# Performance work log

Hardware: AMD Instinct MI355X
Metric: run time of the kernel (lower is better)

Reference implementation:

```python
import jax, jax.numpy as jnp
import numpy as np

TOKENS = 64
IN_F = 8192
OUT_F = 8192
CODESZ = 8
CB_SIZE = 256


def fwht(x):
    """Sylvester fast Walsh-Hadamard transform along last dim. x: (B, n), n power of 2."""
    b, n = x.shape
    h = 1
    while h < n:
        x = x.reshape(b, n // (2 * h), 2, h)
        x = jnp.concatenate([x[:, :, :1] + x[:, :, 1:], x[:, :, :1] - x[:, :, 1:]], axis=2)
        x = x.reshape(b, n)
        h *= 2
    return x


def setup_inputs() -> dict:
    key = jax.random.key(0)
    k0, k1, k2, k3, k4, k5 = jax.random.split(key, 6)
    x = jax.random.normal(k0, (TOKENS, IN_F), jnp.float32)
    # SU/SV are random sign vectors in QuIP
    SU = jnp.sign(jax.random.normal(k1, (IN_F,), jnp.float32))
    SV = jnp.sign(jax.random.normal(k2, (OUT_F,), jnp.float32))
    grid = jax.random.normal(k3, (CB_SIZE, CODESZ), jnp.float32)  # codebook entries
    Wscale = jnp.ones((1,), jnp.float32)
    bias = jax.random.normal(k4, (OUT_F,), jnp.float32) * 0.01
    Qidxs = jax.random.randint(k5, (OUT_F, IN_F // CODESZ), 0, CB_SIZE, jnp.int32)
    return {"x": x, "SU": SU, "SV": SV, "grid": grid, "Wscale": Wscale, "bias": bias, "Qidxs": Qidxs}


def reference(x, SU, SV, grid, Wscale, bias, Qidxs):
    # 1) input sign scale
    xs = x * SU
    # 2) matmul_hadUt with folded wscale: x @ H^T / sqrt(n_in) * wscale (H symmetric Sylvester)
    inv_sqrt_in = 1.0 / jnp.sqrt(jnp.asarray(IN_F, x.dtype))
    xh = fwht(xs) * (inv_sqrt_in * Wscale[0])
    # 3) codebook dequant + matmul: W_hat[o, i] from codebook lookup, out = xh @ W_hat^T
    W_hat = grid[Qidxs].reshape(OUT_F, IN_F)  # (out, in) dequantized weight
    y = xh @ W_hat.T  # (tokens, out)
    # 4) matmul_hadU on the output side, truncate to out_features (no-op here: q_out == out)
    inv_sqrt_out = 1.0 / jnp.sqrt(jnp.asarray(OUT_F, x.dtype))
    yh = fwht(y) * inv_sqrt_out
    yh = yh[..., :OUT_F]
    # 5) output sign scale + bias
    return yh * SV + bias
```

## Files before the change

kernel.cpp:

```cpp
#include <hip/hip_runtime.h>
#include <hip/hip_bf16.h>

#define TOKENS 64
#define IN_F 8192
#define OUT_F 8192
#define CB 256

typedef _Float16 half8 __attribute__((ext_vector_type(8)));
typedef float f32x4 __attribute__((ext_vector_type(4)));

__global__ __launch_bounds__(256) void k_fwht_in(const float* __restrict__ x,
                                                 const float* __restrict__ SU,
                                                 const float* __restrict__ Wscale,
                                                 _Float16* __restrict__ xh_frag)
{
    __shared__ float buf[256 * 33];
    __shared__ _Float16 xrowP[256 * 40];
    const int t    = threadIdx.x;
    const int lane = t & 63;
    const int w    = t >> 6;
    const int row  = blockIdx.x;

    float v[32];
    const float* xr = x + row * IN_F;
#pragma unroll
    for (int r = 0; r < 32; ++r) {
        int e = r * 256 + t;
        v[r] = xr[e] * SU[e];
    }
#pragma unroll
    for (int h = 1; h < 32; h <<= 1) {
#pragma unroll
        for (int r = 0; r < 32; ++r) {
            if ((r & h) == 0) {
                float a = v[r], b = v[r + h];
                v[r] = a + b;
                v[r + h] = a - b;
            }
        }
    }
#pragma unroll
    for (int m = 1; m < 64; m <<= 1) {
        bool upper = (lane & m) != 0;
#pragma unroll
        for (int r = 0; r < 32; ++r) {
            float p = __shfl_xor(v[r], m, 64);
            v[r] = upper ? (p - v[r]) : (v[r] + p);
        }
    }
#pragma unroll
    for (int r = 0; r < 32; ++r) buf[t * 33 + r] = v[r];
    __syncthreads();
    {
        float s1 = (w & 1) ? -1.f : 1.f;
        float s2 = (w & 2) ? -1.f : 1.f;
        float s3 = s1 * s2;
#pragma unroll
        for (int r = 0; r < 32; ++r) {
            float a0 = buf[(0 * 64 + lane) * 33 + r];
            float a1 = buf[(1 * 64 + lane) * 33 + r];
            float a2 = buf[(2 * 64 + lane) * 33 + r];
            float a3 = buf[(3 * 64 + lane) * 33 + r];
            v[r] = a0 + s1 * a1 + s2 * a2 + s3 * a3;
        }
    }
    const float scale = 0.011048543456039806f * Wscale[0];
#pragma unroll
    for (int r = 0; r < 32; ++r) {
        int idx = (t & 31) + (r * 8 + (t >> 5)) * 40;
        xrowP[idx] = (_Float16)(v[r] * scale);
    }
    __syncthreads();
    {
        const int mt  = row >> 4;
        const int l15 = row & 15;
        _Float16* base = xh_frag + ((size_t)(t * 4 + mt) * 64 + l15) * 8;
#pragma unroll
        for (int g = 0; g < 4; ++g) {
            half8 val = *(const half8*)&xrowP[t * 40 + g * 8];
            *(half8*)(base + g * 16 * 8) = val;
        }
    }
}

#define SQ_STRIDE 261
__global__ __launch_bounds__(256, 2) void k_qgemm(const _Float16* __restrict__ xh_frag,
                                                  const int* __restrict__ Qidxs,
                                                  const float* __restrict__ grid,
                                                  float* __restrict__ y_part)
{
    __shared__ __align__(16) _Float16 glds[CB * 8];
    __shared__ __align__(16) char uni[4 * 64 * 68 * 4];
    int*   sq  = (int*)uni;
    float* red = (float*)uni;

    const int tid = threadIdx.x;
    const int g   = blockIdx.x >> 2;
    const int p   = blockIdx.x & 3;
    const int n0  = g * 64;

    {
        const float4* gp = (const float4*)grid + tid * 2;
        float4 g0 = gp[0];
        float4 g1 = gp[1];
        _Float16* gl = &glds[tid * 8];
        gl[0] = (_Float16)g0.x; gl[1] = (_Float16)g0.y;
        gl[2] = (_Float16)g0.z; gl[3] = (_Float16)g0.w;
        gl[4] = (_Float16)g1.x; gl[5] = (_Float16)g1.y;
        gl[6] = (_Float16)g1.z; gl[7] = (_Float16)g1.w;
    }
#pragma unroll
    for (int i = 0; i < 16; ++i) {
        int idx4 = i * 256 + tid;
        int r  = idx4 >> 6;
        int c4 = idx4 & 63;
        int4 vv = *(const int4*)(Qidxs + (size_t)(n0 + r) * 1024 + p * 256 + c4 * 4);
        int* dst = &sq[r * SQ_STRIDE + c4 * 4];
        dst[0] = vv.x; dst[1] = vv.y; dst[2] = vv.z; dst[3] = vv.w;
    }
    __syncthreads();

    const int lane = tid & 63;
    const int w    = tid >> 6;
    const int col  = lane & 15;
    const int quad = lane >> 4;

    const int cbase = w * 64 + quad;
#define QGATHER(dst4, s)                                              \
    {                                                                 \
        int cc = cbase + (s) * 4;                                     \
        dst4.x = sq[(0 * 16 + col) * SQ_STRIDE + cc];                 \
        dst4.y = sq[(1 * 16 + col) * SQ_STRIDE + cc];                 \
        dst4.z = sq[(2 * 16 + col) * SQ_STRIDE + cc];                 \
        dst4.w = sq[(3 * 16 + col) * SQ_STRIDE + cc];                 \
    }

    const _Float16* abase = xh_frag + ((size_t)(p * 64 + w * 16) * 4 * 64 + lane) * 8;

    f32x4 acc[4][4] = {};

    int4 qv1, qv2;
    half8 b_c[4];
    {
        int4 qv0;
        QGATHER(qv0, 0);
        QGATHER(qv1, 1);
        QGATHER(qv2, 2);
        b_c[0] = *(const half8*)&glds[qv0.x * 8];
        b_c[1] = *(const half8*)&glds[qv0.y * 8];
        b_c[2] = *(const half8*)&glds[qv0.z * 8];
        b_c[3] = *(const half8*)&glds[qv0.w * 8];
    }
    half8 a_c[4], a_n[4];
#pragma unroll
    for (int mt = 0; mt < 4; ++mt) {
        a_c[mt] = *(const half8*)(abase + (size_t)(0 * 4 + mt) * 512);
        a_n[mt] = *(const half8*)(abase + (size_t)(1 * 4 + mt) * 512);
    }

#pragma unroll 4
    for (int s = 0; s < 16; ++s) {
        const int s3 = (s + 3 < 16 ? s + 3 : 15);
        const int s2 = (s + 2 < 16 ? s + 2 : 15);
        int4 qn;
        QGATHER(qn, s3);
        half8 b_n[4], a_nn[4];
        b_n[0] = *(const half8*)&glds[qv1.x * 8];
        b_n[1] = *(const half8*)&glds[qv1.y * 8];
        b_n[2] = *(const half8*)&glds[qv1.z * 8];
        b_n[3] = *(const half8*)&glds[qv1.w * 8];
#pragma unroll
        for (int mt = 0; mt < 4; ++mt)
            a_nn[mt] = *(const half8*)(abase + (size_t)(s2 * 4 + mt) * 512);
#pragma unroll
        for (int nt = 0; nt < 4; ++nt)
#pragma unroll
            for (int mt = 0; mt < 4; ++mt)
                acc[nt][mt] = __builtin_amdgcn_mfma_f32_16x16x32_f16(
                    a_c[mt], b_c[nt], acc[nt][mt], 0, 0, 0);
#pragma unroll
        for (int nt = 0; nt < 4; ++nt) b_c[nt] = b_n[nt];
        qv1 = qv2; qv2 = qn;
#pragma unroll
        for (int mt = 0; mt < 4; ++mt) { a_c[mt] = a_n[mt]; a_n[mt] = a_nn[mt]; }
    }

    __syncthreads();
#pragma unroll
    for (int nt = 0; nt < 4; ++nt)
#pragma unroll
        for (int mt = 0; mt < 4; ++mt)
#pragma unroll
            for (int i = 0; i < 4; ++i) {
                int r = mt * 16 + quad * 4 + i;
                int c = nt * 16 + col;
                red[(w * 64 + r) * 68 + c] = acc[nt][mt][i];
            }
    __syncthreads();
    float* yp = y_part + (size_t)p * TOKENS * OUT_F;
#pragma unroll
    for (int j = 0; j < 16; ++j) {
        int idx = j * 256 + tid;
        int rr = idx >> 6, cc = idx & 63;
        float s = (red[(0 * 64 + rr) * 68 + cc] + red[(1 * 64 + rr) * 68 + cc])
                + (red[(2 * 64 + rr) * 68 + cc] + red[(3 * 64 + rr) * 68 + cc]);
        yp[(size_t)rr * OUT_F + n0 + cc] = s;
    }
#undef QGATHER
}

__global__ __launch_bounds__(256) void k_fwht_out(const float* __restrict__ y_part,
                                                  const float* __restrict__ SV,
                                                  const float* __restrict__ bias,
                                                  float* __restrict__ out)
{
    __shared__ float buf[256 * 33];
    const int t    = threadIdx.x;
    const int lane = t & 63;
    const int w    = t >> 6;
    const int row  = blockIdx.x;

    const float* y0 = y_part + (size_t)row * OUT_F;
    const size_t ps = (size_t)TOKENS * OUT_F;

    float v[32];
#pragma unroll
    for (int r = 0; r < 32; ++r) {
        int e = r * 256 + t;
        v[r] = (y0[e] + y0[e + ps]) + (y0[e + 2 * ps] + y0[e + 3 * ps]);
    }
#pragma unroll
    for (int h = 1; h < 32; h <<= 1) {
#pragma unroll
        for (int r = 0; r < 32; ++r) {
            if ((r & h) == 0) {
                float a = v[r], b = v[r + h];
                v[r] = a + b;
                v[r + h] = a - b;
            }
        }
    }
#pragma unroll
    for (int m = 1; m < 64; m <<= 1) {
        bool upper = (lane & m) != 0;
#pragma unroll
        for (int r = 0; r < 32; ++r) {
            float p = __shfl_xor(v[r], m, 64);
            v[r] = upper ? (p - v[r]) : (v[r] + p);
        }
    }
#pragma unroll
    for (int r = 0; r < 32; ++r) buf[t * 33 + r] = v[r];
    __syncthreads();
    {
        float s1 = (w & 1) ? -1.f : 1.f;
        float s2 = (w & 2) ? -1.f : 1.f;
        float s3 = s1 * s2;
#pragma unroll
        for (int r = 0; r < 32; ++r) {
            float a0 = buf[(0 * 64 + lane) * 33 + r];
            float a1 = buf[(1 * 64 + lane) * 33 + r];
            float a2 = buf[(2 * 64 + lane) * 33 + r];
            float a3 = buf[(3 * 64 + lane) * 33 + r];
            v[r] = a0 + s1 * a1 + s2 * a2 + s3 * a3;
        }
    }
    const float scale = 0.011048543456039806f;
    float* oo = out + (size_t)row * OUT_F;
#pragma unroll
    for (int r = 0; r < 32; ++r) {
        int e = r * 256 + t;
        oo[e] = v[r] * scale * SV[e] + bias[e];
    }
}

extern "C" void kernel_launch(void* const* d_in, const int* in_sizes, int n_in,
                              void* d_out, int out_size, void* d_ws, size_t ws_size,
                              hipStream_t stream) {
    const float* x      = (const float*)d_in[0];
    const float* SU     = (const float*)d_in[1];
    const float* SV     = (const float*)d_in[2];
    const float* grid   = (const float*)d_in[3];
    const float* Wscale = (const float*)d_in[4];
    const float* bias   = (const float*)d_in[5];
    const int*   Qidxs  = (const int*)d_in[6];
    float* out = (float*)d_out;

    _Float16* xh_frag = (_Float16*)d_ws;
    float*    y_part  = (float*)((char*)d_ws + ((size_t)1 << 20));

    k_fwht_in<<<TOKENS, 256, 0, stream>>>(x, SU, Wscale, xh_frag);
    k_qgemm<<<512, 256, 0, stream>>>(xh_frag, Qidxs, grid, y_part);
    k_fwht_out<<<TOKENS, 256, 0, stream>>>(y_part, SV, bias, out);
}
```

Measured before the change: 113.0 us.

## Split K eight ways in codebook GEMM with u16 index staging and halved LDS

The quantized GEMM's K dimension is split into 8 partitions instead of 4, doubling the grid to 1024 blocks with half the K work per block. Staged indices are stored as 16-bit in LDS and the cross-wave reduction buffer is processed in two halves, shrinking shared memory so the launch bound can request 4 blocks per CU. The goal is more occupancy and parallelism on a latency-bound GEMM. In exchange, partial-sum traffic to global memory doubles and the output FWHT kernel must sum 8 partials, adding an extra reduction sync phase.

```diff
diff --git a/kernel.cpp b/kernel.cpp
--- a/kernel.cpp
+++ b/kernel.cpp
@@ -83,20 +83,20 @@
     }
 }
 
-#define SQ_STRIDE 261
-__global__ __launch_bounds__(256, 2) void k_qgemm(const _Float16* __restrict__ xh_frag,
+#define SQ_U16_STRIDE 130
+__global__ __launch_bounds__(256, 4) void k_qgemm(const _Float16* __restrict__ xh_frag,
                                                   const int* __restrict__ Qidxs,
                                                   const float* __restrict__ grid,
                                                   float* __restrict__ y_part)
 {
     __shared__ __align__(16) _Float16 glds[CB * 8];
-    __shared__ __align__(16) char uni[4 * 64 * 68 * 4];
-    int*   sq  = (int*)uni;
-    float* red = (float*)uni;
+    __shared__ __align__(16) char uni[4 * 64 * 34 * 4];
+    unsigned short* squ = (unsigned short*)uni;
+    float*          red = (float*)uni;
 
     const int tid = threadIdx.x;
-    const int g   = blockIdx.x >> 2;
-    const int p   = blockIdx.x & 3;
+    const int g   = blockIdx.x >> 3;
+    const int p   = blockIdx.x & 7;
     const int n0  = g * 64;
 
     {
@@ -110,13 +110,14 @@
         gl[6] = (_Float16)g1.z; gl[7] = (_Float16)g1.w;
     }
 #pragma unroll
-    for (int i = 0; i < 16; ++i) {
+    for (int i = 0; i < 8; ++i) {
         int idx4 = i * 256 + tid;
-        int r  = idx4 >> 6;
-        int c4 = idx4 & 63;
-        int4 vv = *(const int4*)(Qidxs + (size_t)(n0 + r) * 1024 + p * 256 + c4 * 4);
-        int* dst = &sq[r * SQ_STRIDE + c4 * 4];
-        dst[0] = vv.x; dst[1] = vv.y; dst[2] = vv.z; dst[3] = vv.w;
+        int r  = idx4 >> 5;
+        int c4 = idx4 & 31;
+        int4 vv = *(const int4*)(Qidxs + (size_t)(n0 + r) * 1024 + p * 128 + c4 * 4);
+        unsigned short* dst = &squ[r * SQ_U16_STRIDE + c4 * 4];
+        dst[0] = (unsigned short)vv.x; dst[1] = (unsigned short)vv.y;
+        dst[2] = (unsigned short)vv.z; dst[3] = (unsigned short)vv.w;
     }
     __syncthreads();
 
@@ -125,17 +126,17 @@
     const int col  = lane & 15;
     const int quad = lane >> 4;
 
-    const int cbase = w * 64 + quad;
-#define QGATHER(dst4, s)                                              \
-    {                                                                 \
-        int cc = cbase + (s) * 4;                                     \
-        dst4.x = sq[(0 * 16 + col) * SQ_STRIDE + cc];                 \
-        dst4.y = sq[(1 * 16 + col) * SQ_STRIDE + cc];                 \
-        dst4.z = sq[(2 * 16 + col) * SQ_STRIDE + cc];                 \
-        dst4.w = sq[(3 * 16 + col) * SQ_STRIDE + cc];                 \
-    }
-
-    const _Float16* abase = xh_frag + ((size_t)(p * 64 + w * 16) * 4 * 64 + lane) * 8;
+    const int cbase = w * 32 + quad;
+#define QGATHER(dst4, s)                                                   \
+    {                                                                      \
+        int cc = cbase + (s) * 4;                                          \
+        dst4.x = (int)squ[(0 * 16 + col) * SQ_U16_STRIDE + cc];            \
+        dst4.y = (int)squ[(1 * 16 + col) * SQ_U16_STRIDE + cc];            \
+        dst4.z = (int)squ[(2 * 16 + col) * SQ_U16_STRIDE + cc];            \
+        dst4.w = (int)squ[(3 * 16 + col) * SQ_U16_STRIDE + cc];            \
+    }
+
+    const _Float16* abase = xh_frag + ((size_t)(p * 32 + w * 8) * 4 * 64 + lane) * 8;
 
     f32x4 acc[4][4] = {};
 
@@ -158,10 +159,10 @@
         a_n[mt] = *(const half8*)(abase + (size_t)(1 * 4 + mt) * 512);
     }
 
-#pragma unroll 4
-    for (int s = 0; s < 16; ++s) {
-        const int s3 = (s + 3 < 16 ? s + 3 : 15);
-        const int s2 = (s + 2 < 16 ? s + 2 : 15);
+#pragma unroll
+    for (int s = 0; s < 8; ++s) {
+        const int s3 = (s + 3 < 8 ? s + 3 : 7);
+        const int s2 = (s + 2 < 8 ? s + 2 : 7);
         int4 qn;
         QGATHER(qn, s3);
         half8 b_n[4], a_nn[4];
@@ -185,26 +186,30 @@
         for (int mt = 0; mt < 4; ++mt) { a_c[mt] = a_n[mt]; a_n[mt] = a_nn[mt]; }
     }
 
-    __syncthreads();
-#pragma unroll
-    for (int nt = 0; nt < 4; ++nt)
-#pragma unroll
-        for (int mt = 0; mt < 4; ++mt)
-#pragma unroll
-            for (int i = 0; i < 4; ++i) {
-                int r = mt * 16 + quad * 4 + i;
-                int c = nt * 16 + col;
-                red[(w * 64 + r) * 68 + c] = acc[nt][mt][i];
-            }
-    __syncthreads();
     float* yp = y_part + (size_t)p * TOKENS * OUT_F;
 #pragma unroll
-    for (int j = 0; j < 16; ++j) {
-        int idx = j * 256 + tid;
-        int rr = idx >> 6, cc = idx & 63;
-        float s = (red[(0 * 64 + rr) * 68 + cc] + red[(1 * 64 + rr) * 68 + cc])
-                + (red[(2 * 64 + rr) * 68 + cc] + red[(3 * 64 + rr) * 68 + cc]);
-        yp[(size_t)rr * OUT_F + n0 + cc] = s;
+    for (int h = 0; h < 2; ++h) {
+        __syncthreads();
+#pragma unroll
+        for (int nt2 = 0; nt2 < 2; ++nt2) {
+            int nt = h * 2 + nt2;
+#pragma unroll
+            for (int mt = 0; mt < 4; ++mt)
+#pragma unroll
+                for (int i = 0; i < 4; ++i) {
+                    int r = mt * 16 + quad * 4 + i;
+                    red[(w * 64 + r) * 34 + nt2 * 16 + col] = acc[nt][mt][i];
+                }
+        }
+        __syncthreads();
+#pragma unroll
+        for (int j = 0; j < 8; ++j) {
+            int idx = j * 256 + tid;
+            int rr = idx >> 5, cc = idx & 31;
+            float s = (red[(0 * 64 + rr) * 34 + cc] + red[(1 * 64 + rr) * 34 + cc])
+                    + (red[(2 * 64 + rr) * 34 + cc] + red[(3 * 64 + rr) * 34 + cc]);
+            yp[(size_t)rr * OUT_F + n0 + h * 32 + cc] = s;
+        }
     }
 #undef QGATHER
 }
@@ -227,7 +232,10 @@
 #pragma unroll
     for (int r = 0; r < 32; ++r) {
         int e = r * 256 + t;
-        v[r] = (y0[e] + y0[e + ps]) + (y0[e + 2 * ps] + y0[e + 3 * ps]);
+        float s = 0.f;
+#pragma unroll
+        for (int q = 0; q < 8; ++q) s += y0[e + q * ps];
+        v[r] = s;
     }
 #pragma unroll
     for (int h = 1; h < 32; h <<= 1) {
@@ -290,6 +298,6 @@
     float*    y_part  = (float*)((char*)d_ws + ((size_t)1 << 20));
 
     k_fwht_in<<<TOKENS, 256, 0, stream>>>(x, SU, Wscale, xh_frag);
-    k_qgemm<<<512, 256, 0, stream>>>(xh_frag, Qidxs, grid, y_part);
+    k_qgemm<<<1024, 256, 0, stream>>>(xh_frag, Qidxs, grid, y_part);
     k_fwht_out<<<TOKENS, 256, 0, stream>>>(y_part, SV, bias, out);
 }
```

Result: slower. 126.3 us (+11.8%).
